# Kernel optimization log

Hardware: AMD Instinct MI355X
Metric: run time of the kernel (lower is better)

The kernel has to match this reference:

```python
import jax, jax.numpy as jnp
import numpy as np

N_NODES = 20000
N_EDGES = 200000
D_IN, D_H1, D_H2, D_OUT = 1433, 1000, 500, 7


def setup_inputs() -> dict:
    key = jax.random.key(0)
    ks = jax.random.split(key, 8)
    features = jax.random.normal(ks[0], (N_NODES, D_IN), dtype=jnp.float32)
    src = jax.random.randint(ks[1], (N_EDGES,), 0, N_NODES)
    dst = jax.random.randint(ks[2], (N_EDGES,), 0, N_NODES)
    W1 = jax.random.normal(ks[3], (D_IN, D_H1), dtype=jnp.float32) * 0.02
    b1 = jnp.zeros((D_H1,), dtype=jnp.float32)
    W2 = jax.random.normal(ks[4], (D_H1, D_H2), dtype=jnp.float32) * 0.02
    b2 = jnp.zeros((D_H2,), dtype=jnp.float32)
    W3 = jax.random.normal(ks[5], (D_H2, D_OUT), dtype=jnp.float32) * 0.02
    b3 = jnp.zeros((D_OUT,), dtype=jnp.float32)
    return {"features": features, "src": src, "dst": dst,
            "W1": W1, "b1": b1, "W2": W2, "b2": b2, "W3": W3, "b3": b3}


def reference(features, src, dst, W1, b1, W2, b2, W3, b3):
    N = features.shape[0]

    def agg(x):  # sum_tensors over incoming neighbors: h_i = sum_{(j->i) in E} x_j
        return jax.ops.segment_sum(x[src], dst, num_segments=N)

    # GCN layer 1: aggregate -> linear -> relu
    x = jax.nn.relu(agg(features) @ W1 + b1)       # [N, 1000]
    # GCN layer 2: aggregate -> linear -> relu (dropout = identity in eval)
    x = jax.nn.relu(agg(x) @ W2 + b2)              # [N, 500]
    # output linear -> relu (dropout = identity in eval)
    x = jax.nn.relu(x @ W3 + b3)                   # [N, 7]
    return x
```

## Files before the change

kernel.cpp:

```cpp
#include <hip/hip_runtime.h>
#include <hip/hip_bf16.h>


#define N_NODES 20000
#define N_EDGES 200000
#define D_IN    1433
#define D_H1    1000
#define D_H2    500
#define D_OUT   7

#define MPAD    20096
#define K1PAD   1472
#define N1PAD   1024
#define K2PAD   1024
#define N2PAD   512
#define H1STR   1008
#define H2STR   504
#define MBLK    157
#define SCAN_N  (N_NODES + 1)
#define SCAN_NB 20

typedef __attribute__((ext_vector_type(8))) short short8;
typedef __attribute__((ext_vector_type(8))) unsigned short ushort8_t;
typedef __attribute__((ext_vector_type(4))) float f32x4;

__device__ __forceinline__ unsigned short bf16_rne(float x) {
    unsigned int u = __float_as_uint(x);
    u = (u + 0x7FFFu + ((u >> 16) & 1u)) >> 16;
    return (unsigned short)u;
}
__device__ __forceinline__ float bf16_up(unsigned short h) {
    return __uint_as_float((unsigned int)h << 16);
}

__device__ __forceinline__ void gl_lds16(const unsigned short* g, unsigned short* lds) {
    __builtin_amdgcn_global_load_lds(
        (const __attribute__((address_space(1))) unsigned int*)g,
        (__attribute__((address_space(3))) unsigned int*)lds, 16, 0, 0);
}

__global__ __launch_bounds__(256) void cast_count(const float* __restrict__ F,
                                                  unsigned int* __restrict__ out,
                                                  const int* __restrict__ dst,
                                                  int* __restrict__ offs) {
    int row = blockIdx.x;
    int t = threadIdx.x;
    int e = row * 256 + t;
    if (e < N_EDGES) atomicAdd(&offs[dst[e] + 1], 1);
    const float* fr = F + (size_t)row * D_IN;
    bool live = row < N_NODES;
    for (int kk = t; kk < K1PAD / 2; kk += 256) {
        int k0 = kk * 2;
        float a = (live && k0     < D_IN) ? fr[k0]     : 0.f;
        float b = (live && k0 + 1 < D_IN) ? fr[k0 + 1] : 0.f;
        out[(size_t)row * (K1PAD / 2) + kk] =
            (unsigned int)bf16_rne(a) | ((unsigned int)bf16_rne(b) << 16);
    }
}

__global__ __launch_bounds__(1024) void scan_part(int* __restrict__ offs,
                                                  int* __restrict__ bsum) {
    __shared__ int wsum[16];
    const int t = threadIdx.x, lane = t & 63, wv = t >> 6;
    int i = blockIdx.x * 1024 + t;
    int v = (i < SCAN_N) ? offs[i] : 0;
    #pragma unroll
    for (int s = 1; s < 64; s <<= 1) {
        int u = __shfl_up(v, s, 64);
        if (lane >= s) v += u;
    }
    if (lane == 63) wsum[wv] = v;
    __syncthreads();
    int prefix = 0;
    for (int k = 0; k < wv; ++k) prefix += wsum[k];
    v += prefix;
    if (i < SCAN_N) offs[i] = v;
    if (t == 1023) bsum[blockIdx.x] = v;
}

__global__ __launch_bounds__(64) void scan_sums(int* __restrict__ bsum) {
    const int t = threadIdx.x;
    int v = (t < SCAN_NB) ? bsum[t] : 0;
    #pragma unroll
    for (int s = 1; s < 64; s <<= 1) {
        int u = __shfl_up(v, s, 64);
        if (t >= s) v += u;
    }
    if (t < SCAN_NB) bsum[t] = v;
}

__global__ __launch_bounds__(1024) void scan_add(int* __restrict__ offs,
                                                 const int* __restrict__ bsum,
                                                 int* __restrict__ cursor) {
    int blk = blockIdx.x;
    int i = blk * 1024 + threadIdx.x;
    int add = blk ? bsum[blk - 1] : 0;
    if (i < SCAN_N) {
        int v = offs[i] + add;
        offs[i] = v;
        if (i < N_NODES) cursor[i] = v;
    }
}

__global__ __launch_bounds__(256) void fill_csr(const int* __restrict__ src,
                                                const int* __restrict__ dst,
                                                int* __restrict__ cursor,
                                                int* __restrict__ srcs) {
    int e = blockIdx.x * 256 + threadIdx.x;
    if (e < N_EDGES) {
        int pos = atomicAdd(&cursor[dst[e]], 1);
        srcs[pos] = src[e];
    }
}

template <int SR, int SC, int DR, int DC>
__global__ __launch_bounds__(256) void transpose_cast_pad(const float* __restrict__ src,
                                                          unsigned short* __restrict__ dst) {
    __shared__ float tile[32][33];
    int c0 = blockIdx.x * 32;
    int r0 = blockIdx.y * 32;
    int tx = threadIdx.x & 31, ty = threadIdx.x >> 5;
    #pragma unroll
    for (int p = 0; p < 4; ++p) {
        int r = r0 + ty + p * 8, c = c0 + tx;
        tile[ty + p * 8][tx] = (r < SR && c < SC) ? src[(size_t)r * SC + c] : 0.f;
    }
    __syncthreads();
    #pragma unroll
    for (int p = 0; p < 4; ++p) {
        int dr = c0 + ty + p * 8;
        int dc = r0 + tx;
        if (dr < DR && dc < DC) dst[(size_t)dr * DC + dc] = bf16_rne(tile[tx][ty + p * 8]);
    }
}

template <int KPAD, int NB>
__global__ __launch_bounds__(256) void gemm_mfma(const unsigned short* __restrict__ A,
                                                 const unsigned short* __restrict__ B,
                                                 unsigned short* __restrict__ C,
                                                 int M, int OSTR) {
    __shared__ __align__(16) unsigned short sA[128 * 64];
    __shared__ __align__(16) unsigned short sB[128 * 64];
    const int bid = blockIdx.x;
    const int xcd = bid & 7;
    const int tt  = bid >> 3;
    const int nb  = tt % NB;
    const int mb  = (tt / NB) * 8 + xcd;
    if (mb >= MBLK) return;

    const int t = threadIdx.x;
    const int w = t >> 6, lane = t & 63;
    const int m0 = mb * 128, n0 = nb * 128;
    const int wm = (w >> 1) * 64, wn = (w & 1) * 64;

    const int srowo = lane >> 3;
    const int skc   = ((lane & 7) ^ srowo) * 8;
    const int mrow = lane & 15, quad = lane >> 4;

    const unsigned short* Aptr = A + (size_t)(m0 + srowo) * KPAD + skc;
    const unsigned short* Bptr = B + (size_t)(n0 + srowo) * KPAD + skc;

    f32x4 acc[4][4] = {};

    for (int k0 = 0; k0 < KPAD; k0 += 64) {
        #pragma unroll
        for (int c = 0; c < 4; ++c) {
            const int rbase = c * 32 + w * 8;
            gl_lds16(Aptr + (size_t)rbase * KPAD, &sA[rbase * 64]);
            gl_lds16(Bptr + (size_t)rbase * KPAD, &sB[rbase * 64]);
        }
        Aptr += 64; Bptr += 64;
        __syncthreads();

        #pragma unroll
        for (int s = 0; s < 2; ++s) {
            short8 af[4], bf[4];
            #pragma unroll
            for (int mt = 0; mt < 4; ++mt) {
                int r = wm + mt * 16 + mrow;
                af[mt] = *(const short8*)&sA[r * 64 + (((s * 4 + quad) ^ (mrow & 7)) * 8)];
            }
            #pragma unroll
            for (int nt = 0; nt < 4; ++nt) {
                int r = wn + nt * 16 + mrow;
                bf[nt] = *(const short8*)&sB[r * 64 + (((s * 4 + quad) ^ (mrow & 7)) * 8)];
            }
            #pragma unroll
            for (int mt = 0; mt < 4; ++mt)
                #pragma unroll
                for (int nt = 0; nt < 4; ++nt)
                    acc[mt][nt] = __builtin_amdgcn_mfma_f32_16x16x32_bf16(
                        af[mt], bf[nt], acc[mt][nt], 0, 0, 0);
        }
        __syncthreads();
    }

    #pragma unroll
    for (int mt = 0; mt < 4; ++mt) {
        int m = m0 + wm + mt * 16 + quad * 4;
        #pragma unroll
        for (int nt = 0; nt < 4; ++nt) {
            int n = n0 + wn + nt * 16 + mrow;
            if (n >= OSTR) continue;
            #pragma unroll
            for (int r = 0; r < 4; ++r)
                if (m + r < M) C[(size_t)(m + r) * OSTR + n] = bf16_rne(acc[mt][nt][r]);
        }
    }
}

__global__ __launch_bounds__(128) void agg1_bf16(const unsigned short* __restrict__ H,
                                                 const int* __restrict__ offs,
                                                 const int* __restrict__ srcs,
                                                 const float* __restrict__ bias,
                                                 unsigned short* __restrict__ X) {
    const int i = blockIdx.x, t = threadIdx.x;
    const bool active = t < 125;
    const int tc = active ? t : 124;
    ushort8_t o = (ushort8_t)0;
    if (i < N_NODES) {
        const int beg = offs[i], end = offs[i + 1];
        const unsigned short* Hc = H + tc * 8;
        float s[8] = {};
        int e = beg;
        for (; e + 8 <= end; e += 8) {
            int j0 = srcs[e],     j1 = srcs[e + 1], j2 = srcs[e + 2], j3 = srcs[e + 3];
            int j4 = srcs[e + 4], j5 = srcs[e + 5], j6 = srcs[e + 6], j7 = srcs[e + 7];
            ushort8_t v0 = *(const ushort8_t*)(Hc + (size_t)j0 * H1STR);
            ushort8_t v1 = *(const ushort8_t*)(Hc + (size_t)j1 * H1STR);
            ushort8_t v2 = *(const ushort8_t*)(Hc + (size_t)j2 * H1STR);
            ushort8_t v3 = *(const ushort8_t*)(Hc + (size_t)j3 * H1STR);
            ushort8_t v4 = *(const ushort8_t*)(Hc + (size_t)j4 * H1STR);
            ushort8_t v5 = *(const ushort8_t*)(Hc + (size_t)j5 * H1STR);
            ushort8_t v6 = *(const ushort8_t*)(Hc + (size_t)j6 * H1STR);
            ushort8_t v7 = *(const ushort8_t*)(Hc + (size_t)j7 * H1STR);
            #pragma unroll
            for (int u = 0; u < 8; ++u) {
                float t0 = (bf16_up(v0[u]) + bf16_up(v1[u])) +
                           (bf16_up(v2[u]) + bf16_up(v3[u]));
                float t1 = (bf16_up(v4[u]) + bf16_up(v5[u])) +
                           (bf16_up(v6[u]) + bf16_up(v7[u]));
                s[u] += t0 + t1;
            }
        }
        for (; e + 4 <= end; e += 4) {
            int j0 = srcs[e], j1 = srcs[e + 1], j2 = srcs[e + 2], j3 = srcs[e + 3];
            ushort8_t v0 = *(const ushort8_t*)(Hc + (size_t)j0 * H1STR);
            ushort8_t v1 = *(const ushort8_t*)(Hc + (size_t)j1 * H1STR);
            ushort8_t v2 = *(const ushort8_t*)(Hc + (size_t)j2 * H1STR);
            ushort8_t v3 = *(const ushort8_t*)(Hc + (size_t)j3 * H1STR);
            #pragma unroll
            for (int u = 0; u < 8; ++u)
                s[u] += (bf16_up(v0[u]) + bf16_up(v1[u])) +
                        (bf16_up(v2[u]) + bf16_up(v3[u]));
        }
        for (; e < end; ++e) {
            ushort8_t v = *(const ushort8_t*)(Hc + (size_t)srcs[e] * H1STR);
            #pragma unroll
            for (int u = 0; u < 8; ++u) s[u] += bf16_up(v[u]);
        }
        if (active) {
            #pragma unroll
            for (int u = 0; u < 8; ++u)
                o[u] = bf16_rne(fmaxf(s[u] + bias[t * 8 + u], 0.f));
        }
    }
    *(ushort8_t*)(X + (size_t)i * K2PAD + t * 8) = o;
}

__global__ __launch_bounds__(64) void agg2_out(const unsigned short* __restrict__ H,
                                               const int* __restrict__ offs,
                                               const int* __restrict__ srcs,
                                               const float* __restrict__ b2,
                                               const float* __restrict__ W3,
                                               const float* __restrict__ b3,
                                               float* __restrict__ out) {
    const int i = blockIdx.x, t = threadIdx.x;
    const int tc = t < 63 ? t : 62;
    const int beg = offs[i], end = offs[i + 1];
    const unsigned short* Hc = H + tc * 8;
    float s[8] = {};
    int e = beg;
    for (; e + 8 <= end; e += 8) {
        int j0 = srcs[e],     j1 = srcs[e + 1], j2 = srcs[e + 2], j3 = srcs[e + 3];
        int j4 = srcs[e + 4], j5 = srcs[e + 5], j6 = srcs[e + 6], j7 = srcs[e + 7];
        ushort8_t v0 = *(const ushort8_t*)(Hc + (size_t)j0 * H2STR);
        ushort8_t v1 = *(const ushort8_t*)(Hc + (size_t)j1 * H2STR);
        ushort8_t v2 = *(const ushort8_t*)(Hc + (size_t)j2 * H2STR);
        ushort8_t v3 = *(const ushort8_t*)(Hc + (size_t)j3 * H2STR);
        ushort8_t v4 = *(const ushort8_t*)(Hc + (size_t)j4 * H2STR);
        ushort8_t v5 = *(const ushort8_t*)(Hc + (size_t)j5 * H2STR);
        ushort8_t v6 = *(const ushort8_t*)(Hc + (size_t)j6 * H2STR);
        ushort8_t v7 = *(const ushort8_t*)(Hc + (size_t)j7 * H2STR);
        #pragma unroll
        for (int u = 0; u < 8; ++u) {
            float t0 = (bf16_up(v0[u]) + bf16_up(v1[u])) +
                       (bf16_up(v2[u]) + bf16_up(v3[u]));
            float t1 = (bf16_up(v4[u]) + bf16_up(v5[u])) +
                       (bf16_up(v6[u]) + bf16_up(v7[u]));
            s[u] += t0 + t1;
        }
    }
    for (; e + 4 <= end; e += 4) {
        int j0 = srcs[e], j1 = srcs[e + 1], j2 = srcs[e + 2], j3 = srcs[e + 3];
        ushort8_t v0 = *(const ushort8_t*)(Hc + (size_t)j0 * H2STR);
        ushort8_t v1 = *(const ushort8_t*)(Hc + (size_t)j1 * H2STR);
        ushort8_t v2 = *(const ushort8_t*)(Hc + (size_t)j2 * H2STR);
        ushort8_t v3 = *(const ushort8_t*)(Hc + (size_t)j3 * H2STR);
        #pragma unroll
        for (int u = 0; u < 8; ++u)
            s[u] += (bf16_up(v0[u]) + bf16_up(v1[u])) +
                    (bf16_up(v2[u]) + bf16_up(v3[u]));
    }
    for (; e < end; ++e) {
        ushort8_t v = *(const ushort8_t*)(Hc + (size_t)srcs[e] * H2STR);
        #pragma unroll
        for (int u = 0; u < 8; ++u) s[u] += bf16_up(v[u]);
    }

    float acc[D_OUT] = {};
    if (t < 63) {
        #pragma unroll
        for (int u = 0; u < 8; ++u) {
            int col = t * 8 + u;
            if (col < D_H2) {
                float x = fmaxf(s[u] + b2[col], 0.f);
                const float* wr = W3 + (size_t)col * D_OUT;
                #pragma unroll
                for (int j = 0; j < D_OUT; ++j) acc[j] += x * wr[j];
            }
        }
    }
    #pragma unroll
    for (int j = 0; j < D_OUT; ++j)
        #pragma unroll
        for (int off = 32; off; off >>= 1) acc[j] += __shfl_down(acc[j], off);
    if (t == 0) {
        #pragma unroll
        for (int j = 0; j < D_OUT; ++j)
            out[(size_t)i * D_OUT + j] = fmaxf(acc[j] + b3[j], 0.f);
    }
}

extern "C" void kernel_launch(void* const* d_in, const int* in_sizes, int n_in,
                              void* d_out, int out_size, void* d_ws, size_t ws_size,
                              hipStream_t stream) {
    const float* features = (const float*)d_in[0];
    const int*   src      = (const int*)d_in[1];
    const int*   dst      = (const int*)d_in[2];
    const float* W1       = (const float*)d_in[3];
    const float* b1       = (const float*)d_in[4];
    const float* W2       = (const float*)d_in[5];
    const float* b2       = (const float*)d_in[6];
    const float* W3       = (const float*)d_in[7];
    const float* b3       = (const float*)d_in[8];
    float* out = (float*)d_out;

    char* ws = (char*)d_ws;
    unsigned short* Fbf  = (unsigned short*)(ws + 0);
    unsigned short* X1bf = (unsigned short*)(ws + 0);
    unsigned short* H1   = (unsigned short*)(ws + 59162624);
    unsigned short* H2   = (unsigned short*)(ws + 59162624);
    unsigned short* W1T  = (unsigned short*)(ws + 99482624);
    unsigned short* W2T  = (unsigned short*)(ws + 102497280);
    int* offs   = (int*)(ws + 103545856);
    int* cursor = (int*)(ws + 103625984);
    int* srcs   = (int*)(ws + 103706112);
    int* bsum   = cursor + N_NODES;

    hipMemsetAsync(offs, 0, (N_NODES + 1) * sizeof(int), stream);

    cast_count<<<MPAD, 256, 0, stream>>>(features, (unsigned int*)Fbf, dst, offs);
    transpose_cast_pad<D_IN, D_H1, N1PAD, K1PAD>
        <<<dim3(N1PAD / 32, K1PAD / 32), 256, 0, stream>>>(W1, W1T);
    transpose_cast_pad<D_H1, D_H2, N2PAD, K2PAD>
        <<<dim3(N2PAD / 32, K2PAD / 32), 256, 0, stream>>>(W2, W2T);

    scan_part<<<SCAN_NB, 1024, 0, stream>>>(offs, bsum);
    scan_sums<<<1, 64, 0, stream>>>(bsum);
    scan_add<<<SCAN_NB, 1024, 0, stream>>>(offs, bsum, cursor);
    fill_csr<<<(N_EDGES + 255) / 256, 256, 0, stream>>>(src, dst, cursor, srcs);

    gemm_mfma<K1PAD, N1PAD / 128><<<8 * (N1PAD / 128) * 20, 256, 0, stream>>>(
        Fbf, W1T, H1, N_NODES, H1STR);
    agg1_bf16<<<MPAD, 128, 0, stream>>>(H1, offs, srcs, b1, X1bf);

    gemm_mfma<K2PAD, N2PAD / 128><<<8 * (N2PAD / 128) * 20, 256, 0, stream>>>(
        X1bf, W2T, H2, N_NODES, H2STR);
    agg2_out<<<N_NODES, 64, 0, stream>>>(H2, offs, srcs, b2, W3, b3, out);
}
```

Baseline: 420.1 us.

## Fuse CSR build into cooperative kernel and merge weight/feature prep kernels

Collapses the memset, count, three scan kernels and fill into a single cooperative-grid kernel with grid syncs, and merges feature cast and both weight transposes into one prep launch. The CSR build is moved after the first GEMM, and buffers are reorganised so its storage overlaps dead weight and padding space. GEMM output strides are padded to multiples of 128 so the column-bound check can be dropped. The intent is to cut launch overhead and small-kernel serialization. In exchange, the first-phase kernels lose their inter-kernel parallelism and outputs carry wider padded rows.

New measurement: 488.4 us. 16.3% more time.

```diff
diff --git a/kernel.cpp b/kernel.cpp
--- a/kernel.cpp
+++ b/kernel.cpp
@@ -1,5 +1,8 @@
 #include <hip/hip_runtime.h>
 #include <hip/hip_bf16.h>
+#include <hip/hip_cooperative_groups.h>
+
+namespace cg = cooperative_groups;
 
 
 #define N_NODES 20000
@@ -14,11 +17,14 @@
 #define N1PAD   1024
 #define K2PAD   1024
 #define N2PAD   512
-#define H1STR   1008
-#define H2STR   504
+#define H1STR   1024
+#define H2STR   512
 #define MBLK    157
 #define SCAN_N  (N_NODES + 1)
-#define SCAN_NB 20
+#define CSR_NB  20
+#define CSR_T   (CSR_NB * 1024)
+#define TB1     ((N1PAD / 32) * (K1PAD / 32))
+#define TB2     ((N2PAD / 32) * (K2PAD / 32))
 
 typedef __attribute__((ext_vector_type(8))) short short8;
 typedef __attribute__((ext_vector_type(8))) unsigned short ushort8_t;
@@ -39,87 +45,39 @@
         (__attribute__((address_space(3))) unsigned int*)lds, 16, 0, 0);
 }
 
-__global__ __launch_bounds__(256) void cast_count(const float* __restrict__ F,
-                                                  unsigned int* __restrict__ out,
-                                                  const int* __restrict__ dst,
-                                                  int* __restrict__ offs) {
-    int row = blockIdx.x;
-    int t = threadIdx.x;
-    int e = row * 256 + t;
-    if (e < N_EDGES) atomicAdd(&offs[dst[e] + 1], 1);
-    const float* fr = F + (size_t)row * D_IN;
-    bool live = row < N_NODES;
-    for (int kk = t; kk < K1PAD / 2; kk += 256) {
-        int k0 = kk * 2;
-        float a = (live && k0     < D_IN) ? fr[k0]     : 0.f;
-        float b = (live && k0 + 1 < D_IN) ? fr[k0 + 1] : 0.f;
-        out[(size_t)row * (K1PAD / 2) + kk] =
-            (unsigned int)bf16_rne(a) | ((unsigned int)bf16_rne(b) << 16);
-    }
-}
-
-__global__ __launch_bounds__(1024) void scan_part(int* __restrict__ offs,
-                                                  int* __restrict__ bsum) {
-    __shared__ int wsum[16];
-    const int t = threadIdx.x, lane = t & 63, wv = t >> 6;
-    int i = blockIdx.x * 1024 + t;
-    int v = (i < SCAN_N) ? offs[i] : 0;
-    #pragma unroll
-    for (int s = 1; s < 64; s <<= 1) {
-        int u = __shfl_up(v, s, 64);
-        if (lane >= s) v += u;
-    }
-    if (lane == 63) wsum[wv] = v;
-    __syncthreads();
-    int prefix = 0;
-    for (int k = 0; k < wv; ++k) prefix += wsum[k];
-    v += prefix;
-    if (i < SCAN_N) offs[i] = v;
-    if (t == 1023) bsum[blockIdx.x] = v;
-}
-
-__global__ __launch_bounds__(64) void scan_sums(int* __restrict__ bsum) {
-    const int t = threadIdx.x;
-    int v = (t < SCAN_NB) ? bsum[t] : 0;
-    #pragma unroll
-    for (int s = 1; s < 64; s <<= 1) {
-        int u = __shfl_up(v, s, 64);
-        if (t >= s) v += u;
-    }
-    if (t < SCAN_NB) bsum[t] = v;
-}
-
-__global__ __launch_bounds__(1024) void scan_add(int* __restrict__ offs,
-                                                 const int* __restrict__ bsum,
-                                                 int* __restrict__ cursor) {
-    int blk = blockIdx.x;
-    int i = blk * 1024 + threadIdx.x;
-    int add = blk ? bsum[blk - 1] : 0;
-    if (i < SCAN_N) {
-        int v = offs[i] + add;
-        offs[i] = v;
-        if (i < N_NODES) cursor[i] = v;
-    }
-}
-
-__global__ __launch_bounds__(256) void fill_csr(const int* __restrict__ src,
-                                                const int* __restrict__ dst,
-                                                int* __restrict__ cursor,
-                                                int* __restrict__ srcs) {
-    int e = blockIdx.x * 256 + threadIdx.x;
-    if (e < N_EDGES) {
-        int pos = atomicAdd(&cursor[dst[e]], 1);
-        srcs[pos] = src[e];
-    }
-}
-
-template <int SR, int SC, int DR, int DC>
-__global__ __launch_bounds__(256) void transpose_cast_pad(const float* __restrict__ src,
-                                                          unsigned short* __restrict__ dst) {
+__global__ __launch_bounds__(256) void prep(const float* __restrict__ F,
+                                            unsigned int* __restrict__ Fout,
+                                            const float* __restrict__ W1,
+                                            unsigned short* __restrict__ W1T,
+                                            const float* __restrict__ W2,
+                                            unsigned short* __restrict__ W2T) {
     __shared__ float tile[32][33];
-    int c0 = blockIdx.x * 32;
-    int r0 = blockIdx.y * 32;
-    int tx = threadIdx.x & 31, ty = threadIdx.x >> 5;
+    const int bid = blockIdx.x, t = threadIdx.x;
+    if (bid < MPAD) {
+        const float* fr = F + (size_t)bid * D_IN;
+        bool live = bid < N_NODES;
+        for (int kk = t; kk < K1PAD / 2; kk += 256) {
+            int k0 = kk * 2;
+            float a = (live && k0     < D_IN) ? fr[k0]     : 0.f;
+            float b = (live && k0 + 1 < D_IN) ? fr[k0 + 1] : 0.f;
+            Fout[(size_t)bid * (K1PAD / 2) + kk] =
+                (unsigned int)bf16_rne(a) | ((unsigned int)bf16_rne(b) << 16);
+        }
+        return;
+    }
+    const float* src; unsigned short* dst;
+    int SR, SC, DR, DC, bx, by;
+    if (bid < MPAD + TB1) {
+        int l = bid - MPAD;
+        bx = l % (N1PAD / 32); by = l / (N1PAD / 32);
+        src = W1; dst = W1T; SR = D_IN; SC = D_H1; DR = N1PAD; DC = K1PAD;
+    } else {
+        int l = bid - MPAD - TB1;
+        bx = l % (N2PAD / 32); by = l / (N2PAD / 32);
+        src = W2; dst = W2T; SR = D_H1; SC = D_H2; DR = N2PAD; DC = K2PAD;
+    }
+    const int c0 = bx * 32, r0 = by * 32;
+    const int tx = t & 31, ty = t >> 5;
     #pragma unroll
     for (int p = 0; p < 4; ++p) {
         int r = r0 + ty + p * 8, c = c0 + tx;
@@ -131,6 +89,64 @@
         int dr = c0 + ty + p * 8;
         int dc = r0 + tx;
         if (dr < DR && dc < DC) dst[(size_t)dr * DC + dc] = bf16_rne(tile[tx][ty + p * 8]);
+    }
+}
+
+__global__ __launch_bounds__(1024) void csr_build(const int* __restrict__ src,
+                                                  const int* __restrict__ dst,
+                                                  int* __restrict__ offs,
+                                                  int* __restrict__ cursor,
+                                                  int* __restrict__ srcs,
+                                                  int* __restrict__ bsum) {
+    cg::grid_group grid = cg::this_grid();
+    __shared__ int wsum[16];
+    const int t = threadIdx.x, bid = blockIdx.x;
+    const int tid = bid * 1024 + t;
+
+    if (tid < SCAN_N) offs[tid] = 0;
+    grid.sync();
+
+    const int4* dst4 = (const int4*)dst;
+    const int4* src4 = (const int4*)src;
+    for (int q = tid; q * 4 < N_EDGES; q += CSR_T) {
+        int4 d = dst4[q];
+        atomicAdd(&offs[d.x + 1], 1);
+        atomicAdd(&offs[d.y + 1], 1);
+        atomicAdd(&offs[d.z + 1], 1);
+        atomicAdd(&offs[d.w + 1], 1);
+    }
+    grid.sync();
+
+    const int lane = t & 63, wv = t >> 6;
+    int v = (tid < SCAN_N) ? offs[tid] : 0;
+    #pragma unroll
+    for (int s = 1; s < 64; s <<= 1) {
+        int u = __shfl_up(v, s, 64);
+        if (lane >= s) v += u;
+    }
+    if (lane == 63) wsum[wv] = v;
+    __syncthreads();
+    int prefix = 0;
+    for (int k = 0; k < wv; ++k) prefix += wsum[k];
+    v += prefix;
+    if (t == 1023) bsum[bid] = v;
+    grid.sync();
+
+    int add = 0;
+    for (int k = 0; k < bid; ++k) add += bsum[k];
+    v += add;
+    if (tid < SCAN_N) offs[tid] = v;
+    if (tid < N_NODES) cursor[tid] = v;
+    grid.sync();
+
+    for (int q = tid; q * 4 < N_EDGES; q += CSR_T) {
+        int4 d = dst4[q];
+        int4 s = src4[q];
+        int p0 = atomicAdd(&cursor[d.x], 1);
+        int p1 = atomicAdd(&cursor[d.y], 1);
+        int p2 = atomicAdd(&cursor[d.z], 1);
+        int p3 = atomicAdd(&cursor[d.w], 1);
+        srcs[p0] = s.x; srcs[p1] = s.y; srcs[p2] = s.z; srcs[p3] = s.w;
     }
 }
 
@@ -201,7 +217,6 @@
         #pragma unroll
         for (int nt = 0; nt < 4; ++nt) {
             int n = n0 + wn + nt * 16 + mrow;
-            if (n >= OSTR) continue;
             #pragma unroll
             for (int r = 0; r < 4; ++r)
                 if (m + r < M) C[(size_t)(m + r) * OSTR + n] = bf16_rne(acc[mt][nt][r]);
@@ -361,31 +376,28 @@
     unsigned short* X1bf = (unsigned short*)(ws + 0);
     unsigned short* H1   = (unsigned short*)(ws + 59162624);
     unsigned short* H2   = (unsigned short*)(ws + 59162624);
-    unsigned short* W1T  = (unsigned short*)(ws + 99482624);
-    unsigned short* W2T  = (unsigned short*)(ws + 102497280);
-    int* offs   = (int*)(ws + 103545856);
-    int* cursor = (int*)(ws + 103625984);
-    int* srcs   = (int*)(ws + 103706112);
-    int* bsum   = cursor + N_NODES;
-
-    hipMemsetAsync(offs, 0, (N_NODES + 1) * sizeof(int), stream);
-
-    cast_count<<<MPAD, 256, 0, stream>>>(features, (unsigned int*)Fbf, dst, offs);
-    transpose_cast_pad<D_IN, D_H1, N1PAD, K1PAD>
-        <<<dim3(N1PAD / 32, K1PAD / 32), 256, 0, stream>>>(W1, W1T);
-    transpose_cast_pad<D_H1, D_H2, N2PAD, K2PAD>
-        <<<dim3(N2PAD / 32, K2PAD / 32), 256, 0, stream>>>(W2, W2T);
-
-    scan_part<<<SCAN_NB, 1024, 0, stream>>>(offs, bsum);
-    scan_sums<<<1, 64, 0, stream>>>(bsum);
-    scan_add<<<SCAN_NB, 1024, 0, stream>>>(offs, bsum, cursor);
-    fill_csr<<<(N_EDGES + 255) / 256, 256, 0, stream>>>(src, dst, cursor, srcs);
+    unsigned short* W1T  = (unsigned short*)(ws + 100122624);
+    unsigned short* W2T  = (unsigned short*)(ws + 103137280);
+    int* offs   = (int*)(ws + 100122624);
+    int* cursor = (int*)(ws + 100202752);
+    int* bsum   = (int*)(ws + 100282752);
+    int* srcs   = (int*)(ws + 100282880);
+
+    prep<<<MPAD + TB1 + TB2, 256, 0, stream>>>(
+        features, (unsigned int*)Fbf, W1, W1T, W2, W2T);
 
     gemm_mfma<K1PAD, N1PAD / 128><<<8 * (N1PAD / 128) * 20, 256, 0, stream>>>(
-        Fbf, W1T, H1, N_NODES, H1STR);
+        Fbf, W1T, H1, N_NODES, N1PAD);
+
+    void* cargs[] = {(void*)&src, (void*)&dst, (void*)&offs,
+                     (void*)&cursor, (void*)&srcs, (void*)&bsum};
+    hipLaunchCooperativeKernel((void*)csr_build, dim3(CSR_NB), dim3(1024),
+                               cargs, 0, stream);
+
     agg1_bf16<<<MPAD, 128, 0, stream>>>(H1, offs, srcs, b1, X1bf);
 
     gemm_mfma<K2PAD, N2PAD / 128><<<8 * (N2PAD / 128) * 20, 256, 0, stream>>>(
-        X1bf, W2T, H2, N_NODES, H2STR);
+        X1bf, W2T, H2, N_NODES, N2PAD);
+
     agg2_out<<<N_NODES, 64, 0, stream>>>(H2, offs, srcs, b2, W3, b3, out);
 }
```
